# Kernel tuning notes

Measured on AMD Instinct MI355X. Metric: run time of the kernel, lower is better.

The kernel has to match this reference:

```python
import jax, jax.numpy as jnp
import numpy as np

N_NODES = 50000
N_EDGES = 800000
D = 128  # policy_input_dim == hidden_dim (required by the original code)


def setup_inputs() -> dict:
    key = jax.random.key(0)
    ks = jax.random.split(key, 16)
    edge_index = jax.random.randint(ks[0], (2, N_EDGES), 0, N_NODES, dtype=jnp.int64)
    # guarantee edge_index.max() + 1 == N_NODES (matches PyG add_self_loops num_nodes)
    edge_index = edge_index.at[:, -1].set(N_NODES - 1)
    edge_attr = jax.random.normal(ks[1], (N_EDGES, D), dtype=jnp.float32)
    s = 1.0 / np.sqrt(D)
    def lin(k):
        kw, kb = jax.random.split(k)
        return (jax.random.uniform(kw, (D, D), jnp.float32, -s, s),
                jax.random.uniform(kb, (D,), jnp.float32, -s, s))
    w1_1, b1_1 = lin(ks[2]); w1_2, b1_2 = lin(ks[3]); w1_out, b1_out = lin(ks[4])
    w2_1, b2_1 = lin(ks[5]); w2_2, b2_2 = lin(ks[6]); w2_out, b2_out = lin(ks[7])
    return {"edge_index": edge_index, "edge_attr": edge_attr,
            "w1_1": w1_1, "b1_1": b1_1, "w1_2": w1_2, "b1_2": b1_2,
            "w1_out": w1_out, "b1_out": b1_out,
            "w2_1": w2_1, "b2_1": b2_1, "w2_2": w2_2, "b2_2": b2_2,
            "w2_out": w2_out, "b2_out": b2_out}


def _conv(edge_index, edge_attr, wa, ba, wb, bb, wo, bo):
    # edge MLP: Linear -> ReLU -> Linear  on edge features [E, D]
    h = jax.nn.relu(edge_attr @ wa + ba) @ wb + bb
    # add_self_loops appends N self-loop edges
    loop = jnp.arange(N_NODES, dtype=edge_index.dtype)
    src = jnp.concatenate([edge_index[0], loop])  # [E+N]
    dst = jnp.concatenate([edge_index[1], loop])
    # PyG lifts edge_attr_j by source node id: gather edge rows by src id
    msg = h[src]  # [E+N, D]
    ssum = jax.ops.segment_sum(msg, dst, num_segments=N_NODES)  # [N, D]
    cnt = jax.ops.segment_sum(jnp.ones((dst.shape[0], 1), h.dtype), dst,
                              num_segments=N_NODES)
    mean = ssum / jnp.maximum(cnt, 1.0)
    return mean @ wo + bo


def reference(edge_index, edge_attr,
              w1_1, b1_1, w1_2, b1_2, w1_out, b1_out,
              w2_1, b2_1, w2_2, b2_2, w2_out, b2_out):
    # conv1 output is computed then discarded by the original module (conv2
    # is fed the raw edge_attr again) — kept here for fidelity.
    x = jax.nn.relu(_conv(edge_index, edge_attr, w1_1, b1_1, w1_2, b1_2, w1_out, b1_out))
    del x
    out = _conv(edge_index, edge_attr, w2_1, b2_1, w2_2, b2_2, w2_out, b2_out)
    return out
```

## Files before the change

kernel.cpp:

```cpp
#include <hip/hip_runtime.h>

#define D 128
#define WPITCH 136
#define TP 132
#define ROWS 64
#define CAP 64

typedef __attribute__((ext_vector_type(8))) short bf16x8;
typedef __attribute__((ext_vector_type(4))) float floatx4;
typedef __attribute__((ext_vector_type(8))) unsigned short ushort8;

__device__ __forceinline__ float bf2f(unsigned short u) {
    union { unsigned int i; float f; } v; v.i = (unsigned int)u << 16; return v.f;
}
__device__ __forceinline__ unsigned short f2bf(float f) {
    unsigned int x = __float_as_uint(f);
    x += 0x7FFF + ((x >> 16) & 1);
    return (unsigned short)(x >> 16);
}

__global__ __launch_bounds__(256) void wt_zero_kernel(
    const float* __restrict__ W1, const float* __restrict__ W2, const float* __restrict__ Wo,
    unsigned short* __restrict__ WT, int* __restrict__ cursor, int N)
{
    if (blockIdx.x >= 6) {
        const int t = (blockIdx.x - 6) * 256 + threadIdx.x;
        if (t < N) cursor[t] = 0;
        return;
    }
    __shared__ unsigned short s[128 * 130];
    const int mi = blockIdx.x >> 1, phase = blockIdx.x & 1;
    const float* W = mi == 0 ? W1 : (mi == 1 ? W2 : Wo);
    unsigned short* out = WT + (mi * 2 + phase) * (D * D);
    for (int i = threadIdx.x; i < D * D; i += 256) {
        const int k = i >> 7, n = i & 127;
        const float w = W[i];
        const unsigned short hb = f2bf(w);
        s[n * 130 + k] = phase ? f2bf(w - bf2f(hb)) : hb;
    }
    __syncthreads();
    for (int i = threadIdx.x; i < D * D; i += 256) {
        const int n = i >> 7, k = i & 127;
        out[i] = s[n * 130 + k];
    }
}

__global__ __launch_bounds__(256) void mlp_kernel(
    const float* __restrict__ X,
    const unsigned short* __restrict__ WT,
    const float* __restrict__ B1, const float* __restrict__ B2,
    float* __restrict__ g, int N)
{
    __shared__ unsigned short sWT[D * WPITCH];
    __shared__ __align__(16) unsigned int sT[ROWS * TP];
    const int tid  = threadIdx.x;
    const int wv   = tid >> 6, lane = tid & 63;
    const int m    = lane & 15, quad = lane >> 4;
    const int r0   = blockIdx.x * ROWS;

    bf16x8 Ah[4], Al[4];
    {
        const float* Xr = X + (size_t)(r0 + wv * 16 + m) * D + quad * 8;
        #pragma unroll
        for (int kc = 0; kc < 4; ++kc) {
            float4 v0 = *(const float4*)(Xr + kc * 32);
            float4 v1 = *(const float4*)(Xr + kc * 32 + 4);
            float xv[8] = {v0.x, v0.y, v0.z, v0.w, v1.x, v1.y, v1.z, v1.w};
            bf16x8 hp, lp;
            #pragma unroll
            for (int j = 0; j < 8; ++j) {
                unsigned short hb = f2bf(xv[j]);
                hp[j] = (short)hb;
                lp[j] = (short)f2bf(xv[j] - bf2f(hb));
            }
            Ah[kc] = hp; Al[kc] = lp;
        }
    }

    for (int L = 0; L < 3; ++L) {
        floatx4 acc[8];
        #pragma unroll
        for (int nt = 0; nt < 8; ++nt) acc[nt] = (floatx4){0.f, 0.f, 0.f, 0.f};
        #pragma unroll
        for (int phase = 0; phase < 2; ++phase) {
            const unsigned short* src = WT + (L * 2 + phase) * (D * D);
            for (int i = tid; i < D * D / 8; i += 256) {
                const int n = i >> 4, k8 = (i & 15) << 3;
                *(ushort8*)&sWT[n * WPITCH + k8] = *(const ushort8*)(src + n * D + k8);
            }
            __syncthreads();
            #pragma unroll
            for (int nt = 0; nt < 8; ++nt) {
                #pragma unroll
                for (int kc = 0; kc < 4; ++kc) {
                    bf16x8 b = *(const bf16x8*)&sWT[(nt * 16 + m) * WPITCH + kc * 32 + quad * 8];
                    acc[nt] = __builtin_amdgcn_mfma_f32_16x16x32_bf16(Ah[kc], b, acc[nt], 0, 0, 0);
                    if (phase == 0)
                        acc[nt] = __builtin_amdgcn_mfma_f32_16x16x32_bf16(Al[kc], b, acc[nt], 0, 0, 0);
                }
            }
            __syncthreads();
        }
        if (L < 2) {
            const float* Bv = (L == 0) ? B1 : B2;
            #pragma unroll
            for (int nt = 0; nt < 8; ++nt) {
                const int col = nt * 16 + m;
                const float bias = Bv[col];
                #pragma unroll
                for (int r = 0; r < 4; ++r) {
                    float v = acc[nt][r] + bias;
                    if (L == 0) v = v > 0.f ? v : 0.f;
                    const unsigned short hb = f2bf(v);
                    const unsigned short lb = f2bf(v - bf2f(hb));
                    sT[(wv * 16 + quad * 4 + r) * TP + col] = ((unsigned int)lb << 16) | hb;
                }
            }
            #pragma unroll
            for (int kc = 0; kc < 4; ++kc) {
                const unsigned int* p = &sT[(wv * 16 + m) * TP + kc * 32 + quad * 8];
                uint4 u0 = *(const uint4*)p, u1 = *(const uint4*)(p + 4);
                unsigned int uu[8] = {u0.x, u0.y, u0.z, u0.w, u1.x, u1.y, u1.z, u1.w};
                bf16x8 hp, lp;
                #pragma unroll
                for (int j = 0; j < 8; ++j) {
                    hp[j] = (short)(uu[j] & 0xFFFFu);
                    lp[j] = (short)(uu[j] >> 16);
                }
                Ah[kc] = hp; Al[kc] = lp;
            }
        } else {
            #pragma unroll
            for (int nt = 0; nt < 8; ++nt) {
                const int col = nt * 16 + m;
                #pragma unroll
                for (int r = 0; r < 4; ++r) {
                    const int grow = r0 + wv * 16 + quad * 4 + r;
                    if (grow < N) g[(size_t)grow * D + col] = acc[nt][r];
                }
            }
        }
    }
}

__global__ __launch_bounds__(256) void fill_kernel(
    const int* __restrict__ src, const int* __restrict__ dst,
    int* __restrict__ cursor, int* __restrict__ adj, int E)
{
    const int e = blockIdx.x * 256 + threadIdx.x;
    if (e >= E) return;
    const int d = dst[e];
    const int pos = atomicAdd(&cursor[d], 1);
    if (pos < CAP) adj[(size_t)d * CAP + pos] = src[e];
}

__global__ __launch_bounds__(256) void gather_kernel(
    const float* __restrict__ g, const int* __restrict__ adj,
    const int* __restrict__ cursor, const float* __restrict__ Bo,
    float* __restrict__ out, int N)
{
    const int wid  = (blockIdx.x * 256 + threadIdx.x) >> 6;
    if (wid >= N) return;
    const int lane = threadIdx.x & 63;
    const int sub  = lane >> 4, li = lane & 15;
    const int degf = cursor[wid];
    const int deg  = degf < CAP ? degf : CAP;
    const float4* gp = (const float4*)g;
    const size_t colo = (size_t)li * 2;
    float4 a0 = {0.f, 0.f, 0.f, 0.f}, a1 = {0.f, 0.f, 0.f, 0.f};
    if (sub == 0) {
        a0 = gp[(size_t)wid * 32 + colo];
        a1 = gp[(size_t)wid * 32 + colo + 1];
    }
    const int* ap = adj + (size_t)wid * CAP;
    int j = sub;
    for (; j + 4 < deg; j += 8) {
        const int s0 = ap[j], s1 = ap[j + 4];
        const float4 v00 = gp[(size_t)s0 * 32 + colo];
        const float4 v01 = gp[(size_t)s0 * 32 + colo + 1];
        const float4 v10 = gp[(size_t)s1 * 32 + colo];
        const float4 v11 = gp[(size_t)s1 * 32 + colo + 1];
        a0.x += v00.x + v10.x; a0.y += v00.y + v10.y;
        a0.z += v00.z + v10.z; a0.w += v00.w + v10.w;
        a1.x += v01.x + v11.x; a1.y += v01.y + v11.y;
        a1.z += v01.z + v11.z; a1.w += v01.w + v11.w;
    }
    for (; j < deg; j += 4) {
        const int s0 = ap[j];
        const float4 v00 = gp[(size_t)s0 * 32 + colo];
        const float4 v01 = gp[(size_t)s0 * 32 + colo + 1];
        a0.x += v00.x; a0.y += v00.y; a0.z += v00.z; a0.w += v00.w;
        a1.x += v01.x; a1.y += v01.y; a1.z += v01.z; a1.w += v01.w;
    }
    #pragma unroll
    for (int off = 16; off <= 32; off <<= 1) {
        a0.x += __shfl_xor(a0.x, off, 64); a0.y += __shfl_xor(a0.y, off, 64);
        a0.z += __shfl_xor(a0.z, off, 64); a0.w += __shfl_xor(a0.w, off, 64);
        a1.x += __shfl_xor(a1.x, off, 64); a1.y += __shfl_xor(a1.y, off, 64);
        a1.z += __shfl_xor(a1.z, off, 64); a1.w += __shfl_xor(a1.w, off, 64);
    }
    if (sub == 0) {
        const float inv = 1.0f / (float)(degf + 1);
        const float4 b0 = ((const float4*)Bo)[colo];
        const float4 b1 = ((const float4*)Bo)[colo + 1];
        float4 o0, o1;
        o0.x = a0.x * inv + b0.x; o0.y = a0.y * inv + b0.y;
        o0.z = a0.z * inv + b0.z; o0.w = a0.w * inv + b0.w;
        o1.x = a1.x * inv + b1.x; o1.y = a1.y * inv + b1.y;
        o1.z = a1.z * inv + b1.z; o1.w = a1.w * inv + b1.w;
        ((float4*)out)[(size_t)wid * 32 + colo]     = o0;
        ((float4*)out)[(size_t)wid * 32 + colo + 1] = o1;
    }
}

extern "C" void kernel_launch(void* const* d_in, const int* in_sizes, int n_in,
                              void* d_out, int out_size, void* d_ws, size_t ws_size,
                              hipStream_t stream) {
    const int*   edge_index = (const int*)d_in[0];
    const float* edge_attr  = (const float*)d_in[1];
    const float* w2_1 = (const float*)d_in[8];
    const float* b2_1 = (const float*)d_in[9];
    const float* w2_2 = (const float*)d_in[10];
    const float* b2_2 = (const float*)d_in[11];
    const float* w2_o = (const float*)d_in[12];
    const float* b2_o = (const float*)d_in[13];

    const int E  = in_sizes[0] / 2;
    const int N  = out_size / D;
    const int NB = (N + ROWS - 1) / ROWS;

    char* p = (char*)d_ws;
    unsigned short* WT = (unsigned short*)p;  p += (size_t)6 * D * D * sizeof(unsigned short);
    float* g           = (float*)p;           p += (size_t)NB * ROWS * D * sizeof(float);
    int*   cursor      = (int*)p;             p += (size_t)N * sizeof(int);
    int*   adj         = (int*)p;

    wt_zero_kernel<<<6 + (N + 255) / 256, 256, 0, stream>>>(w2_1, w2_2, w2_o, WT, cursor, N);
    fill_kernel<<<(E + 255) / 256, 256, 0, stream>>>(
        edge_index, edge_index + E, cursor, adj, E);
    mlp_kernel<<<NB, 256, 0, stream>>>(edge_attr, WT, b2_1, b2_2, g, N);
    gather_kernel<<<(N * 64 + 255) / 256, 256, 0, stream>>>(
        g, adj, cursor, b2_o, (float*)d_out, N);
}
```

Before: 615.0 us.

## Store g in column-block layout and gather per 16-column block across a 2D grid

The MLP output g is now written in a column-blocked layout: 8 planes of 16 columns, each plane holding all padded rows. The gather kernel launches a 2D grid with one y-index per column block. Each wave loads the adjacency list once, broadcasts source ids with shuffles, and has 16 groups of 4 lanes fetch 64-byte rows in parallel. The goal is to shrink the per-plane working set so it stays L2-resident during random gathers and to get more edges in flight per wave. The cost is that each node's adjacency list is read 8 times, and the output is written in small 64-byte pieces.

```diff
diff --git a/kernel.cpp b/kernel.cpp
--- a/kernel.cpp
+++ b/kernel.cpp
@@ -5,6 +5,8 @@
 #define TP 132
 #define ROWS 64
 #define CAP 64
+#define CB 16
+#define NCB (D / CB)
 
 typedef __attribute__((ext_vector_type(8))) short bf16x8;
 typedef __attribute__((ext_vector_type(4))) float floatx4;
@@ -57,6 +59,7 @@
     const int wv   = tid >> 6, lane = tid & 63;
     const int m    = lane & 15, quad = lane >> 4;
     const int r0   = blockIdx.x * ROWS;
+    const size_t cbstride = (size_t)gridDim.x * ROWS * CB;
 
     bf16x8 Ah[4], Al[4];
     {
@@ -132,11 +135,10 @@
         } else {
             #pragma unroll
             for (int nt = 0; nt < 8; ++nt) {
-                const int col = nt * 16 + m;
                 #pragma unroll
                 for (int r = 0; r < 4; ++r) {
                     const int grow = r0 + wv * 16 + quad * 4 + r;
-                    if (grow < N) g[(size_t)grow * D + col] = acc[nt][r];
+                    g[(size_t)nt * cbstride + (size_t)grow * CB + m] = acc[nt][r];
                 }
             }
         }
@@ -155,61 +157,52 @@
 }
 
 __global__ __launch_bounds__(256) void gather_kernel(
-    const float* __restrict__ g, const int* __restrict__ adj,
-    const int* __restrict__ cursor, const float* __restrict__ Bo,
-    float* __restrict__ out, int N)
-{
-    const int wid  = (blockIdx.x * 256 + threadIdx.x) >> 6;
-    if (wid >= N) return;
+    const float* __restrict__ g,
+    const int* __restrict__ adj,
+    const int* __restrict__ cursor,
+    const float* __restrict__ Bo,
+    float* __restrict__ out, int N, int Npad)
+{
+    const int node = (blockIdx.x * 256 + threadIdx.x) >> 6;
+    if (node >= N) return;
+    const int cb   = blockIdx.y;
     const int lane = threadIdx.x & 63;
-    const int sub  = lane >> 4, li = lane & 15;
-    const int degf = cursor[wid];
+    const int grp  = lane >> 2, li = lane & 3;
+
+    const int degf = __builtin_nontemporal_load(&cursor[node]);
     const int deg  = degf < CAP ? degf : CAP;
-    const float4* gp = (const float4*)g;
-    const size_t colo = (size_t)li * 2;
-    float4 a0 = {0.f, 0.f, 0.f, 0.f}, a1 = {0.f, 0.f, 0.f, 0.f};
-    if (sub == 0) {
-        a0 = gp[(size_t)wid * 32 + colo];
-        a1 = gp[(size_t)wid * 32 + colo + 1];
-    }
-    const int* ap = adj + (size_t)wid * CAP;
-    int j = sub;
-    for (; j + 4 < deg; j += 8) {
-        const int s0 = ap[j], s1 = ap[j + 4];
-        const float4 v00 = gp[(size_t)s0 * 32 + colo];
-        const float4 v01 = gp[(size_t)s0 * 32 + colo + 1];
-        const float4 v10 = gp[(size_t)s1 * 32 + colo];
-        const float4 v11 = gp[(size_t)s1 * 32 + colo + 1];
-        a0.x += v00.x + v10.x; a0.y += v00.y + v10.y;
-        a0.z += v00.z + v10.z; a0.w += v00.w + v10.w;
-        a1.x += v01.x + v11.x; a1.y += v01.y + v11.y;
-        a1.z += v01.z + v11.z; a1.w += v01.w + v11.w;
-    }
-    for (; j < deg; j += 4) {
-        const int s0 = ap[j];
-        const float4 v00 = gp[(size_t)s0 * 32 + colo];
-        const float4 v01 = gp[(size_t)s0 * 32 + colo + 1];
-        a0.x += v00.x; a0.y += v00.y; a0.z += v00.z; a0.w += v00.w;
-        a1.x += v01.x; a1.y += v01.y; a1.z += v01.z; a1.w += v01.w;
+    const float* gcb = g + (size_t)cb * Npad * CB;
+
+    int ai = 0;
+    if (lane < deg) ai = __builtin_nontemporal_load(&adj[(size_t)node * CAP + lane]);
+
+    floatx4 a = {0.f, 0.f, 0.f, 0.f};
+    if (lane < 4) {
+        a = ((const floatx4*)(gcb + (size_t)node * CB))[lane];
+    }
+    const int nk = (deg + 15) >> 4;
+    for (int k = 0; k < nk; ++k) {
+        const int j = grp + (k << 4);
+        const int s = __shfl(ai, j, 64);
+        if (j < deg) {
+            const floatx4 v = ((const floatx4*)(gcb + (size_t)s * CB))[li];
+            a.x += v.x; a.y += v.y; a.z += v.z; a.w += v.w;
+        }
     }
     #pragma unroll
-    for (int off = 16; off <= 32; off <<= 1) {
-        a0.x += __shfl_xor(a0.x, off, 64); a0.y += __shfl_xor(a0.y, off, 64);
-        a0.z += __shfl_xor(a0.z, off, 64); a0.w += __shfl_xor(a0.w, off, 64);
-        a1.x += __shfl_xor(a1.x, off, 64); a1.y += __shfl_xor(a1.y, off, 64);
-        a1.z += __shfl_xor(a1.z, off, 64); a1.w += __shfl_xor(a1.w, off, 64);
-    }
-    if (sub == 0) {
+    for (int off = 4; off <= 32; off <<= 1) {
+        a.x += __shfl_xor(a.x, off, 64);
+        a.y += __shfl_xor(a.y, off, 64);
+        a.z += __shfl_xor(a.z, off, 64);
+        a.w += __shfl_xor(a.w, off, 64);
+    }
+    if (lane < 4) {
         const float inv = 1.0f / (float)(degf + 1);
-        const float4 b0 = ((const float4*)Bo)[colo];
-        const float4 b1 = ((const float4*)Bo)[colo + 1];
-        float4 o0, o1;
-        o0.x = a0.x * inv + b0.x; o0.y = a0.y * inv + b0.y;
-        o0.z = a0.z * inv + b0.z; o0.w = a0.w * inv + b0.w;
-        o1.x = a1.x * inv + b1.x; o1.y = a1.y * inv + b1.y;
-        o1.z = a1.z * inv + b1.z; o1.w = a1.w * inv + b1.w;
-        ((float4*)out)[(size_t)wid * 32 + colo]     = o0;
-        ((float4*)out)[(size_t)wid * 32 + colo + 1] = o1;
+        const floatx4 b = ((const floatx4*)Bo)[cb * 4 + lane];
+        floatx4 o;
+        o.x = a.x * inv + b.x; o.y = a.y * inv + b.y;
+        o.z = a.z * inv + b.z; o.w = a.w * inv + b.w;
+        __builtin_nontemporal_store(o, (floatx4*)out + (size_t)node * (D / 4) + cb * 4 + lane);
     }
 }
 
@@ -225,13 +218,14 @@
     const float* w2_o = (const float*)d_in[12];
     const float* b2_o = (const float*)d_in[13];
 
-    const int E  = in_sizes[0] / 2;
-    const int N  = out_size / D;
-    const int NB = (N + ROWS - 1) / ROWS;
+    const int E    = in_sizes[0] / 2;
+    const int N    = out_size / D;
+    const int NB   = (N + ROWS - 1) / ROWS;
+    const int Npad = NB * ROWS;
 
     char* p = (char*)d_ws;
     unsigned short* WT = (unsigned short*)p;  p += (size_t)6 * D * D * sizeof(unsigned short);
-    float* g           = (float*)p;           p += (size_t)NB * ROWS * D * sizeof(float);
+    float* g           = (float*)p;           p += (size_t)Npad * D * sizeof(float);
     int*   cursor      = (int*)p;             p += (size_t)N * sizeof(int);
     int*   adj         = (int*)p;
 
@@ -239,6 +233,6 @@
     fill_kernel<<<(E + 255) / 256, 256, 0, stream>>>(
         edge_index, edge_index + E, cursor, adj, E);
     mlp_kernel<<<NB, 256, 0, stream>>>(edge_attr, WT, b2_1, b2_2, g, N);
-    gather_kernel<<<(N * 64 + 255) / 256, 256, 0, stream>>>(
-        g, adj, cursor, b2_o, (float*)d_out, N);
-}
+    gather_kernel<<<dim3((N + 3) / 4, NCB), 256, 0, stream>>>(
+        g, adj, cursor, b2_o, (float*)d_out, N, Npad);
+}
```

New measurement: 699.9 us. 1.14x slower.

## Merge adjacency fill into MLP kernel launch and use nontemporal output stores

Applied to the files above, without the earlier changes.

Folds the edge-bucketing fill kernel into the MLP kernel as extra trailing blocks, so the atomic-heavy fill work can run alongside the MFMA-bound MLP blocks and one launch is dropped. The gather kernel's final output writes become nontemporal stores to avoid polluting cache. The fused kernel carries the MLP's large shared-memory footprint for the fill blocks too, which may limit how many fill blocks are resident at once.

```diff
diff --git a/kernel.cpp b/kernel.cpp
--- a/kernel.cpp
+++ b/kernel.cpp
@@ -45,12 +45,23 @@
     }
 }
 
-__global__ __launch_bounds__(256) void mlp_kernel(
+__global__ __launch_bounds__(256) void mlp_fill_kernel(
     const float* __restrict__ X,
     const unsigned short* __restrict__ WT,
     const float* __restrict__ B1, const float* __restrict__ B2,
-    float* __restrict__ g, int N)
+    float* __restrict__ g, int N, int NB,
+    const int* __restrict__ esrc, const int* __restrict__ edst,
+    int* __restrict__ cursor, int* __restrict__ adj, int E)
 {
+    if ((int)blockIdx.x >= NB) {
+        const int e = ((int)blockIdx.x - NB) * 256 + threadIdx.x;
+        if (e < E) {
+            const int d = edst[e];
+            const int pos = atomicAdd(&cursor[d], 1);
+            if (pos < CAP) adj[(size_t)d * CAP + pos] = esrc[e];
+        }
+        return;
+    }
     __shared__ unsigned short sWT[D * WPITCH];
     __shared__ __align__(16) unsigned int sT[ROWS * TP];
     const int tid  = threadIdx.x;
@@ -141,17 +152,6 @@
             }
         }
     }
-}
-
-__global__ __launch_bounds__(256) void fill_kernel(
-    const int* __restrict__ src, const int* __restrict__ dst,
-    int* __restrict__ cursor, int* __restrict__ adj, int E)
-{
-    const int e = blockIdx.x * 256 + threadIdx.x;
-    if (e >= E) return;
-    const int d = dst[e];
-    const int pos = atomicAdd(&cursor[d], 1);
-    if (pos < CAP) adj[(size_t)d * CAP + pos] = src[e];
 }
 
 __global__ __launch_bounds__(256) void gather_kernel(
@@ -203,13 +203,13 @@
         const float inv = 1.0f / (float)(degf + 1);
         const float4 b0 = ((const float4*)Bo)[colo];
         const float4 b1 = ((const float4*)Bo)[colo + 1];
-        float4 o0, o1;
+        floatx4 o0, o1;
         o0.x = a0.x * inv + b0.x; o0.y = a0.y * inv + b0.y;
         o0.z = a0.z * inv + b0.z; o0.w = a0.w * inv + b0.w;
         o1.x = a1.x * inv + b1.x; o1.y = a1.y * inv + b1.y;
         o1.z = a1.z * inv + b1.z; o1.w = a1.w * inv + b1.w;
-        ((float4*)out)[(size_t)wid * 32 + colo]     = o0;
-        ((float4*)out)[(size_t)wid * 32 + colo + 1] = o1;
+        __builtin_nontemporal_store(o0, (floatx4*)out + (size_t)wid * 32 + colo);
+        __builtin_nontemporal_store(o1, (floatx4*)out + (size_t)wid * 32 + colo + 1);
     }
 }
 
@@ -228,6 +228,7 @@
     const int E  = in_sizes[0] / 2;
     const int N  = out_size / D;
     const int NB = (N + ROWS - 1) / ROWS;
+    const int FB = (E + 255) / 256;
 
     char* p = (char*)d_ws;
     unsigned short* WT = (unsigned short*)p;  p += (size_t)6 * D * D * sizeof(unsigned short);
@@ -236,9 +237,9 @@
     int*   adj         = (int*)p;
 
     wt_zero_kernel<<<6 + (N + 255) / 256, 256, 0, stream>>>(w2_1, w2_2, w2_o, WT, cursor, N);
-    fill_kernel<<<(E + 255) / 256, 256, 0, stream>>>(
+    mlp_fill_kernel<<<NB + FB, 256, 0, stream>>>(
+        edge_attr, WT, b2_1, b2_2, g, N, NB,
         edge_index, edge_index + E, cursor, adj, E);
-    mlp_kernel<<<NB, 256, 0, stream>>>(edge_attr, WT, b2_1, b2_2, g, N);
     gather_kernel<<<(N * 64 + 255) / 256, 256, 0, stream>>>(
         g, adj, cursor, b2_o, (float*)d_out, N);
 }
```

Result: faster. 590.6 us (-4.0%).
